# Kernel optimization log

Measured on AMD Instinct MI355X. Metric: run time of the kernel, lower is better.

## Reference

```python
import jax, jax.numpy as jnp
import numpy as np

N = 100_000   # nodes
E = 3_200_000 # edges (avg degree 32)

def _glorot(k, shape):
    fan_in, fan_out = shape
    lim = float(np.sqrt(6.0 / (fan_in + fan_out)))
    return jax.random.uniform(k, shape, jnp.float32, -lim, lim)

def setup_inputs() -> dict:
    key = jax.random.key(0)
    ks = jax.random.split(key, 8)
    x = jax.random.normal(ks[0], (N, 3), dtype=jnp.float32)
    edge_index = jax.random.randint(ks[1], (2, E), 0, N, dtype=jnp.int32)
    choices = jax.random.bernoulli(ks[2], 0.5, (N,))
    W1 = _glorot(ks[3], (3, 16));  b1 = jnp.zeros((16,), jnp.float32)
    W2 = _glorot(ks[4], (16, 16)); b2 = jnp.zeros((16,), jnp.float32)
    W3 = _glorot(ks[5], (16, 1));  b3 = jnp.zeros((1,), jnp.float32)
    fc_w = _glorot(ks[6], (16, 1)); fc_b = jnp.zeros((1,), jnp.float32)
    return dict(x=x, edge_index=edge_index, choices=choices,
                W1=W1, b1=b1, W2=W2, b2=b2, W3=W3, b3=b3,
                fc_w=fc_w, fc_b=fc_b)

def reference(x, edge_index, choices, W1, b1, W2, b2, W3, b3, fc_w, fc_b):
    row, col = edge_index[0], edge_index[1]  # source -> target
    # improved=True GCN norm: self-loop weight 2, deg = in_degree + 2
    deg = jax.ops.segment_sum(jnp.ones((E,), x.dtype), col, num_segments=N) + 2.0
    dinv = jax.lax.rsqrt(deg)                    # [N]
    enorm = dinv[row] * dinv[col]                # [E] edge normalization
    self_norm = 2.0 * dinv * dinv                # [N] self-loop term

    def gcn(h, W, b):
        h = h @ W                                # [N, F_out]
        agg = jax.ops.segment_sum(h[row] * enorm[:, None], col, num_segments=N)
        return agg + self_norm[:, None] * h + b

    h = jax.nn.relu(gcn(x, W1, b1))
    h = jax.nn.relu(gcn(h, W2, b2))
    c = gcn(h, W3, b3)[:, 0]                     # [N] per-node logit
    # masked softmax over chosen nodes (torch masked_select + softmax,
    # expressed with static shape: non-chosen entries get probability 0)
    logits = jnp.where(choices, c, -jnp.inf)
    choice = jax.nn.softmax(logits, axis=0)      # [N]
    # global_mean_pool with a single graph = mean over all nodes
    v = jnp.mean(h, axis=0, keepdims=True)       # [1, 16]
    value = v @ fc_w + fc_b                      # [1, 1]
    return choice, value
```

## Files before the change

kernel.cpp:

```cpp
#include <hip/hip_runtime.h>
#include <hip/hip_fp16.h>
#include <math.h>

#define BLK 256


#define BSH 8
#define NB 512
#define CAP 10240
#define SCAP 11264
#define EB 8192
#define BINTH 512

__device__ inline float4 load_h4(const __half* base, int node, int sub) {
    const uint2* p = reinterpret_cast<const uint2*>(base + ((size_t)node << 4)) + sub;
    uint2 u = *p;
    union { unsigned u; __half2 h; } a, b;
    a.u = u.x; b.u = u.y;
    float2 fa = __half22float2(a.h), fb = __half22float2(b.h);
    return make_float4(fa.x, fa.y, fb.x, fb.y);
}

__device__ inline void store_h4(__half* base, int node, int sub, float4 v) {
    union { unsigned u; __half2 h; } a, b;
    a.h = __floats2half2_rn(v.x, v.y);
    b.h = __floats2half2_rn(v.z, v.w);
    uint2 u; u.x = a.u; u.y = b.u;
    *(reinterpret_cast<uint2*>(base + ((size_t)node << 4)) + sub) = u;
}

__device__ inline float3 load_xs(const __half* xs, int node) {
    uint2 u = *reinterpret_cast<const uint2*>(xs + ((size_t)node << 2));
    union { unsigned u; __half2 h; } a, b;
    a.u = u.x; b.u = u.y;
    float2 fa = __half22float2(a.h), fb = __half22float2(b.h);
    return make_float3(fa.x, fa.y, fb.x);
}

__global__ void k_init(int* __restrict__ gcur, float* __restrict__ scal) {
    int t = threadIdx.x;
    gcur[t] = 0;
    if (t < 18) scal[t] = 0.f;
}

__global__ void __launch_bounds__(BINTH) k_bin(const int* __restrict__ row,
                                               const int* __restrict__ col,
                                               int* __restrict__ gcur,
                                               int* __restrict__ packed, int E) {
    __shared__ int stage[EB];
    __shared__ unsigned short sbuk[EB];
    __shared__ int hist[NB];
    __shared__ int lscan[NB];
    __shared__ int cur[NB];
    __shared__ int gbase[NB];
    int tid = threadIdx.x;
    int base = blockIdx.x * EB;
    int cnt = min(EB, E - base);

    hist[tid] = 0;
    __syncthreads();
    for (int j = tid; j < cnt; j += BINTH) {
        int c = __builtin_nontemporal_load(col + base + j);
        atomicAdd(&hist[c >> BSH], 1);
    }
    __syncthreads();
    lscan[tid] = hist[tid];
    __syncthreads();
    for (int d = 1; d < NB; d <<= 1) {
        int t = (tid >= d) ? lscan[tid - d] : 0;
        __syncthreads();
        if (tid >= d) lscan[tid] += t;
        __syncthreads();
    }
    {
        int ex = lscan[tid] - hist[tid];
        lscan[tid] = ex;
        cur[tid] = ex;
    }
    __syncthreads();
    for (int j = tid; j < cnt; j += BINTH) {
        int c = __builtin_nontemporal_load(col + base + j);
        int r = __builtin_nontemporal_load(row + base + j);
        int b = c >> BSH;
        int p = atomicAdd(&cur[b], 1);
        stage[p] = (r << BSH) | (c & ((1 << BSH) - 1));
        sbuk[p] = (unsigned short)b;
    }
    __syncthreads();
    if (hist[tid] > 0) gbase[tid] = tid * CAP + atomicAdd(&gcur[tid], hist[tid]);
    __syncthreads();
    for (int j = tid; j < cnt; j += BINTH) {
        int b = sbuk[j];
        int pos = gbase[b] + (j - lscan[b]);
        packed[pos] = stage[j];
    }
}

__global__ void __launch_bounds__(BLK) k_place(const int* __restrict__ packed,
                                               const int* __restrict__ bcnt,
                                               const float* __restrict__ x,
                                               int* __restrict__ degi,
                                               int* __restrict__ offs,
                                               float* __restrict__ dinv,
                                               __half* __restrict__ xs,
                                               int* __restrict__ srcs, int n) {
    __shared__ int cnt[256];
    __shared__ int lcur[256];
    __shared__ int ssum[256];
    int tid = threadIdx.x;
    int b = blockIdx.x;
    int nb0 = b << BSH;
    cnt[tid] = 0;
    __syncthreads();
    int ecnt = bcnt[b];
    const int* pk = packed + (size_t)b * CAP;
    for (int j = tid; j < ecnt; j += BLK)
        atomicAdd(&cnt[pk[j] & 255], 1);
    __syncthreads();
    int c = cnt[tid];
    int pl = (c + 3) & ~3;
    ssum[tid] = pl;
    __syncthreads();
    for (int d = 1; d < 256; d <<= 1) {
        int t = (tid >= d) ? ssum[tid - d] : 0;
        __syncthreads();
        if (tid >= d) ssum[tid] += t;
        __syncthreads();
    }
    int A = b * SCAP + (ssum[tid] - pl);
    lcur[tid] = A;
    int valid = min(n - nb0, 256);
    int i = nb0 + tid;
    if (tid < valid) {
        degi[i] = pl;
        offs[i] = A;
        float di = rsqrtf((float)c + 2.0f);
        dinv[i] = di;
        float x0 = x[i * 3 + 0], x1 = x[i * 3 + 1], x2 = x[i * 3 + 2];
        union { unsigned u; __half2 h; } a2, b2;
        a2.h = __floats2half2_rn(di * x0, di * x1);
        b2.h = __floats2half2_rn(di * x2, 0.f);
        uint2 u; u.x = a2.u; u.y = b2.u;
        *reinterpret_cast<uint2*>(xs + ((size_t)i << 2)) = u;
        for (int k = c; k < pl; k++) srcs[A + k] = n;
    }
    if (b == 0 && tid == 0) {
        uint2 z; z.x = 0u; z.y = 0u;
        *reinterpret_cast<uint2*>(xs + ((size_t)n << 2)) = z;
    }
    __syncthreads();
    for (int j = tid; j < ecnt; j += BLK) {
        int v = pk[j];
        int li = v & 255;
        int slot = atomicAdd(&lcur[li], 1);
        srcs[slot] = v >> BSH;
    }
}

__global__ void __launch_bounds__(BLK) k_agg1(const __half* __restrict__ xs,
                                              const int* __restrict__ offs,
                                              const int* __restrict__ degi,
                                              const int* __restrict__ srcs,
                                              const float* __restrict__ dinv,
                                              const float* __restrict__ b1,
                                              const float* __restrict__ W1,
                                              const float* __restrict__ W2,
                                              __half* __restrict__ hwsB, int n) {
    __shared__ float w1[48];
    __shared__ float w2[256];
    __shared__ float bb[16];
    __shared__ float hbuf[64][17];
    int tid = threadIdx.x;
    w2[tid] = W2[tid];
    if (tid < 48) w1[tid] = W1[tid];
    if (tid < 16) bb[tid] = b1[tid];
    if (blockIdx.x == 0 && tid < 8)
        reinterpret_cast<unsigned*>(hwsB + ((size_t)n << 4))[tid] = 0u;
    __syncthreads();
    int nl = tid >> 2, sub = tid & 3;
    int i = blockIdx.x * 64 + nl;
    bool act = (i < n);
    float di = 0.f;
    if (act) {
        di = dinv[i];
        float ax = 0.f, ay = 0.f, az = 0.f;
        float bx = 0.f, by = 0.f, bz = 0.f;
        int A = offs[i], pc = degi[i];
        for (int j = A + 4 * sub; j < A + pc; j += 16) {
            int4 s = *reinterpret_cast<const int4*>(srcs + j);
            float3 q0 = load_xs(xs, s.x);
            float3 q1 = load_xs(xs, s.y);
            float3 q2 = load_xs(xs, s.z);
            float3 q3 = load_xs(xs, s.w);
            ax += q0.x + q1.x; ay += q0.y + q1.y; az += q0.z + q1.z;
            bx += q2.x + q3.x; by += q2.y + q3.y; bz += q2.z + q3.z;
        }
        ax += bx; ay += by; az += bz;
        ax += __shfl_xor(ax, 1); ay += __shfl_xor(ay, 1); az += __shfl_xor(az, 1);
        ax += __shfl_xor(ax, 2); ay += __shfl_xor(ay, 2); az += __shfl_xor(az, 2);
        float3 s = load_xs(xs, i);
        ax += 2.f * s.x; ay += 2.f * s.y; az += 2.f * s.z;
#pragma unroll
        for (int k = 0; k < 4; k++) {
            int f = sub * 4 + k;
            float hv = di * (ax * w1[f] + ay * w1[16 + f] + az * w1[32 + f]) + bb[f];
            hbuf[nl][f] = fmaxf(hv, 0.f);
        }
    }
    __syncthreads();
    if (act) {
        const float* hn = hbuf[nl];
        float s0 = 0.f, s1 = 0.f, s2 = 0.f, s3 = 0.f;
#pragma unroll
        for (int f = 0; f < 16; f++) {
            float hv = hn[f];
            const float4 wq = *(const float4*)&w2[f * 16 + sub * 4];
            s0 += hv * wq.x; s1 += hv * wq.y; s2 += hv * wq.z; s3 += hv * wq.w;
        }
        store_h4(hwsB, i, sub, make_float4(di * s0, di * s1, di * s2, di * s3));
    }
}

#define GATHERV(HWS)                                                            \
    float4 acc;                                                                 \
    {                                                                           \
        float4 s0 = load_h4(HWS, i, sub);                                       \
        acc = make_float4(2.f * s0.x, 2.f * s0.y, 2.f * s0.z, 2.f * s0.w);      \
        float4 a1 = make_float4(0.f, 0.f, 0.f, 0.f);                            \
        float4 a2 = a1, a3 = a1;                                                \
        int A = offs[i], pc = degi[i];                                          \
        int j = A;                                                              \
        for (; j + 8 <= A + pc; j += 8) {                                       \
            int4 sa = *reinterpret_cast<const int4*>(srcs + j);                 \
            int4 sb = *reinterpret_cast<const int4*>(srcs + j + 4);             \
            float4 q0 = load_h4(HWS, sa.x, sub);                                \
            float4 q1 = load_h4(HWS, sa.y, sub);                                \
            float4 q2 = load_h4(HWS, sa.z, sub);                                \
            float4 q3 = load_h4(HWS, sa.w, sub);                                \
            float4 q4 = load_h4(HWS, sb.x, sub);                                \
            float4 q5 = load_h4(HWS, sb.y, sub);                                \
            float4 q6 = load_h4(HWS, sb.z, sub);                                \
            float4 q7 = load_h4(HWS, sb.w, sub);                                \
            acc.x += q0.x + q4.x; acc.y += q0.y + q4.y;                         \
            acc.z += q0.z + q4.z; acc.w += q0.w + q4.w;                         \
            a1.x += q1.x + q5.x; a1.y += q1.y + q5.y;                           \
            a1.z += q1.z + q5.z; a1.w += q1.w + q5.w;                           \
            a2.x += q2.x + q6.x; a2.y += q2.y + q6.y;                           \
            a2.z += q2.z + q6.z; a2.w += q2.w + q6.w;                           \
            a3.x += q3.x + q7.x; a3.y += q3.y + q7.y;                           \
            a3.z += q3.z + q7.z; a3.w += q3.w + q7.w;                           \
        }                                                                       \
        if (j < A + pc) {                   \
            int4 sa = *reinterpret_cast<const int4*>(srcs + j);                 \
            float4 q0 = load_h4(HWS, sa.x, sub);                                \
            float4 q1 = load_h4(HWS, sa.y, sub);                                \
            float4 q2 = load_h4(HWS, sa.z, sub);                                \
            float4 q3 = load_h4(HWS, sa.w, sub);                                \
            acc.x += q0.x; acc.y += q0.y; acc.z += q0.z; acc.w += q0.w;         \
            a1.x += q1.x; a1.y += q1.y; a1.z += q1.z; a1.w += q1.w;             \
            a2.x += q2.x; a2.y += q2.y; a2.z += q2.z; a2.w += q2.w;             \
            a3.x += q3.x; a3.y += q3.y; a3.z += q3.z; a3.w += q3.w;             \
        }                                                                       \
        acc.x += a1.x + a2.x + a3.x;                                            \
        acc.y += a1.y + a2.y + a3.y;                                            \
        acc.z += a1.z + a2.z + a3.z;                                            \
        acc.w += a1.w + a2.w + a3.w;                                            \
    }

__global__ void __launch_bounds__(BLK) k_agg2(const __half* __restrict__ hwsB,
                                              const int* __restrict__ offs,
                                              const int* __restrict__ degi,
                                              const int* __restrict__ srcs,
                                              const float* __restrict__ dinv,
                                              const float* __restrict__ b2,
                                              const float* __restrict__ W3,
                                              float* __restrict__ hws3,
                                              float* __restrict__ pool, int n) {
    __shared__ float w3[16];
    __shared__ float bb[16];
    __shared__ float lp[16];
    int tid = threadIdx.x;
    if (tid < 16) { w3[tid] = W3[tid]; bb[tid] = b2[tid]; lp[tid] = 0.f; }
    if (blockIdx.x == 0 && tid == 0) hws3[n] = 0.f;
    __syncthreads();
    int nl = tid >> 2, sub = tid & 3;
    int i = blockIdx.x * 64 + nl;
    bool act = (i < n);
    float4 h = make_float4(0.f, 0.f, 0.f, 0.f);
    if (act) {
        float di = dinv[i];
        GATHERV(hwsB);
        h.x = fmaxf(di * acc.x + bb[sub * 4 + 0], 0.f);
        h.y = fmaxf(di * acc.y + bb[sub * 4 + 1], 0.f);
        h.z = fmaxf(di * acc.z + bb[sub * 4 + 2], 0.f);
        h.w = fmaxf(di * acc.w + bb[sub * 4 + 3], 0.f);
        float p = h.x * w3[sub * 4 + 0] + h.y * w3[sub * 4 + 1]
                + h.z * w3[sub * 4 + 2] + h.w * w3[sub * 4 + 3];
        p += __shfl_xor(p, 1);
        p += __shfl_xor(p, 2);
        if (sub == 0) hws3[i] = di * p;
    }
    float4 hp = h;
#pragma unroll
    for (int m = 4; m < 64; m <<= 1) {
        hp.x += __shfl_xor(hp.x, m);
        hp.y += __shfl_xor(hp.y, m);
        hp.z += __shfl_xor(hp.z, m);
        hp.w += __shfl_xor(hp.w, m);
    }
    if ((tid & 63) < 4) {
        atomicAdd(&lp[sub * 4 + 0], hp.x);
        atomicAdd(&lp[sub * 4 + 1], hp.y);
        atomicAdd(&lp[sub * 4 + 2], hp.z);
        atomicAdd(&lp[sub * 4 + 3], hp.w);
    }
    __syncthreads();
    if (tid < 16) atomicAdd(&pool[tid], lp[tid]);
}

__global__ void __launch_bounds__(BLK) k_agg3(const float* __restrict__ hws3,
                                              const int* __restrict__ offs,
                                              const int* __restrict__ degi,
                                              const int* __restrict__ srcs,
                                              const float* __restrict__ dinv,
                                              const float* __restrict__ b3,
                                              const int* __restrict__ choices,
                                              float* __restrict__ cbuf,
                                              float* __restrict__ bmax,
                                              float* __restrict__ bsum, int n) {
    __shared__ float red[BLK];
    int tid = threadIdx.x;
    int nl = tid >> 2, sub = tid & 3;
    int i = blockIdx.x * 64 + nl;
    bool act = (i < n);
    float s0 = 0.f, s1 = 0.f;
    if (act) {
        int A = offs[i], pc = degi[i];
        for (int j = A + 4 * sub; j < A + pc; j += 16) {
            int4 s = *reinterpret_cast<const int4*>(srcs + j);
            s0 += hws3[s.x] + hws3[s.z];
            s1 += hws3[s.y] + hws3[s.w];
        }
    }
    float s = s0 + s1;
    s += __shfl_xor(s, 1);
    s += __shfl_xor(s, 2);
    float logit = -INFINITY;
    if (act && sub == 0) {
        float c = dinv[i] * (s + 2.f * hws3[i]) + b3[0];
        cbuf[i] = c;
        if (choices[i] != 0) logit = c;
    }
    red[tid] = logit;
    __syncthreads();
    for (int d = BLK / 2; d > 0; d >>= 1) {
        if (tid < d) red[tid] = fmaxf(red[tid], red[tid + d]);
        __syncthreads();
    }
    float bm = red[0];
    __syncthreads();
    red[tid] = (logit > -INFINITY) ? expf(logit - bm) : 0.f;
    __syncthreads();
    for (int d = BLK / 2; d > 0; d >>= 1) {
        if (tid < d) red[tid] += red[tid + d];
        __syncthreads();
    }
    if (tid == 0) { bmax[blockIdx.x] = bm; bsum[blockIdx.x] = red[0]; }
}

__global__ void __launch_bounds__(BLK) k_comb(const float* __restrict__ bmax,
                                              const float* __restrict__ bsum,
                                              float* __restrict__ scal_m,
                                              float* __restrict__ Ssum, int nblk) {
    __shared__ float red[BLK];
    int tid = threadIdx.x;
    float m = -INFINITY;
    for (int i = tid; i < nblk; i += BLK) m = fmaxf(m, bmax[i]);
    red[tid] = m;
    __syncthreads();
    for (int d = BLK / 2; d > 0; d >>= 1) {
        if (tid < d) red[tid] = fmaxf(red[tid], red[tid + d]);
        __syncthreads();
    }
    float M = red[0];
    __syncthreads();
    float s = 0.f;
    for (int i = tid; i < nblk; i += BLK) {
        float bm = bmax[i];
        if (bm > -INFINITY) s += bsum[i] * expf(bm - M);
    }
    red[tid] = s;
    __syncthreads();
    for (int d = BLK / 2; d > 0; d >>= 1) {
        if (tid < d) red[tid] += red[tid + d];
        __syncthreads();
    }
    if (tid == 0) { scal_m[0] = M; Ssum[0] = red[0]; }
}

__global__ void __launch_bounds__(BLK) k_final(const float* __restrict__ cbuf,
                                               const int* __restrict__ choices,
                                               const float* __restrict__ scal_m,
                                               const float* __restrict__ Ssum,
                                               const float* __restrict__ pool,
                                               const float* __restrict__ fcw,
                                               const float* __restrict__ fcb,
                                               float* __restrict__ out, int n) {
    int i = blockIdx.x * BLK + threadIdx.x;
    if (i < n) {
        float p = 0.0f;
        if (choices[i] != 0) {
            float m = scal_m[0], S = Ssum[0];
            p = expf(cbuf[i] - m) / S;
        }
        out[i] = p;
    }
    if (blockIdx.x == 0 && threadIdx.x == 0) {
        float invn = 1.0f / (float)n;
        float v = 0.0f;
#pragma unroll
        for (int f = 0; f < 16; f++) v += (pool[f] * invn) * fcw[f];
        out[n] = v + fcb[0];
    }
}

extern "C" void kernel_launch(void* const* d_in, const int* in_sizes, int n_in,
                              void* d_out, int out_size, void* d_ws, size_t ws_size,
                              hipStream_t stream) {
    const float* x       = (const float*)d_in[0];
    const int*   ei      = (const int*)d_in[1];
    const int*   choices = (const int*)d_in[2];
    const float* W1 = (const float*)d_in[3];
    const float* b1 = (const float*)d_in[4];
    const float* W2 = (const float*)d_in[5];
    const float* b2 = (const float*)d_in[6];
    const float* W3 = (const float*)d_in[7];
    const float* b3 = (const float*)d_in[8];
    const float* fcw = (const float*)d_in[9];
    const float* fcb = (const float*)d_in[10];
    float* out = (float*)d_out;

    int n = in_sizes[0] / 3;
    int E = in_sizes[1] / 2;
    const int* row = ei;
    const int* col = ei + E;

    int nblkN = (n + BLK - 1) / BLK;
    int nblk64 = (n + 63) / 64;
    int nbuck = (n + (1 << BSH) - 1) >> BSH;
    int nblkBin = (E + EB - 1) / EB;

    char* ws = (char*)d_ws;
    size_t o = 0;
    auto alloc = [&](size_t bytes) { char* p = ws + o; o += (bytes + 15) & ~(size_t)15; return p; };
    int*   degi   = (int*)  alloc((size_t)n * 4);
    int*   offs   = (int*)  alloc((size_t)n * 4);
    float* dinv   = (float*)alloc((size_t)n * 4);
    float* hws3   = (float*)alloc((size_t)(n + 1) * 4);
    float* cbuf   = (float*)alloc((size_t)n * 4);
    float* bmax   = (float*)alloc(8192);
    float* bsum   = (float*)alloc(8192);
    int*   gcur   = (int*)  alloc(NB * 4);
    float* scal   = (float*)alloc(256);
    float* Ssum   = scal + 0;
    float* pool   = scal + 1;
    float* scal_m = scal + 17;
    __half* xs    = (__half*)alloc((size_t)(n + 1) * 4 * 2);
    size_t hw_bytes = (size_t)(n + 1) * 16 * 2;
    size_t pk_bytes = (size_t)NB * CAP * 4;
    char*  blob   = alloc(hw_bytes > pk_bytes ? hw_bytes : pk_bytes);
    int*    packed = (int*)blob;
    __half* hwsB   = (__half*)blob;
    int*   srcs   = (int*)  alloc((size_t)NB * SCAP * 4);
    (void)ws_size;

    k_init<<<1, NB, 0, stream>>>(gcur, scal);
    k_bin<<<nblkBin, BINTH, 0, stream>>>(row, col, gcur, packed, E);
    k_place<<<nbuck, BLK, 0, stream>>>(packed, gcur, x, degi, offs, dinv, xs, srcs, n);

    k_agg1<<<nblk64, BLK, 0, stream>>>(xs, offs, degi, srcs, dinv, b1, W1, W2, hwsB, n);
    k_agg2<<<nblk64, BLK, 0, stream>>>(hwsB, offs, degi, srcs, dinv, b2, W3, hws3, pool, n);
    k_agg3<<<nblk64, BLK, 0, stream>>>(hws3, offs, degi, srcs, dinv, b3, choices, cbuf, bmax, bsum, n);

    k_comb<<<1, BLK, 0, stream>>>(bmax, bsum, scal_m, Ssum, nblk64);
    k_final<<<nblkN, BLK, 0, stream>>>(cbuf, choices, scal_m, Ssum, pool, fcw, fcb, out, n);
}
```

Measured before the change: 232.8 us.

## Process two nodes per thread group in aggregation and fold softmax combine into final

Aggregation kernels for layers 2 and 3 now handle two nodes per 4-lane group. Their gather loops are interleaved with sentinel padding so that more independent loads are in flight per thread. Neighbor lists are padded to multiples of 8, with a larger per-bucket capacity, so the 8-wide loop needs no tail handling. The separate single-block softmax combine kernel is removed, and every block of the final kernel recomputes the global max and sum itself. This saves one launch at the cost of redundant per-block reduction work and extra padded gathers.

```diff
diff --git a/kernel.cpp b/kernel.cpp
--- a/kernel.cpp
+++ b/kernel.cpp
@@ -8,7 +8,7 @@
 #define BSH 8
 #define NB 512
 #define CAP 10240
-#define SCAP 11264
+#define SCAP 12288
 #define EB 8192
 #define BINTH 512
 
@@ -118,7 +118,7 @@
         atomicAdd(&cnt[pk[j] & 255], 1);
     __syncthreads();
     int c = cnt[tid];
-    int pl = (c + 3) & ~3;
+    int pl = (c + 7) & ~7;
     ssum[tid] = pl;
     __syncthreads();
     for (int d = 1; d < 256; d <<= 1) {
@@ -221,52 +221,6 @@
     }
 }
 
-#define GATHERV(HWS)                                                            \
-    float4 acc;                                                                 \
-    {                                                                           \
-        float4 s0 = load_h4(HWS, i, sub);                                       \
-        acc = make_float4(2.f * s0.x, 2.f * s0.y, 2.f * s0.z, 2.f * s0.w);      \
-        float4 a1 = make_float4(0.f, 0.f, 0.f, 0.f);                            \
-        float4 a2 = a1, a3 = a1;                                                \
-        int A = offs[i], pc = degi[i];                                          \
-        int j = A;                                                              \
-        for (; j + 8 <= A + pc; j += 8) {                                       \
-            int4 sa = *reinterpret_cast<const int4*>(srcs + j);                 \
-            int4 sb = *reinterpret_cast<const int4*>(srcs + j + 4);             \
-            float4 q0 = load_h4(HWS, sa.x, sub);                                \
-            float4 q1 = load_h4(HWS, sa.y, sub);                                \
-            float4 q2 = load_h4(HWS, sa.z, sub);                                \
-            float4 q3 = load_h4(HWS, sa.w, sub);                                \
-            float4 q4 = load_h4(HWS, sb.x, sub);                                \
-            float4 q5 = load_h4(HWS, sb.y, sub);                                \
-            float4 q6 = load_h4(HWS, sb.z, sub);                                \
-            float4 q7 = load_h4(HWS, sb.w, sub);                                \
-            acc.x += q0.x + q4.x; acc.y += q0.y + q4.y;                         \
-            acc.z += q0.z + q4.z; acc.w += q0.w + q4.w;                         \
-            a1.x += q1.x + q5.x; a1.y += q1.y + q5.y;                           \
-            a1.z += q1.z + q5.z; a1.w += q1.w + q5.w;                           \
-            a2.x += q2.x + q6.x; a2.y += q2.y + q6.y;                           \
-            a2.z += q2.z + q6.z; a2.w += q2.w + q6.w;                           \
-            a3.x += q3.x + q7.x; a3.y += q3.y + q7.y;                           \
-            a3.z += q3.z + q7.z; a3.w += q3.w + q7.w;                           \
-        }                                                                       \
-        if (j < A + pc) {                   \
-            int4 sa = *reinterpret_cast<const int4*>(srcs + j);                 \
-            float4 q0 = load_h4(HWS, sa.x, sub);                                \
-            float4 q1 = load_h4(HWS, sa.y, sub);                                \
-            float4 q2 = load_h4(HWS, sa.z, sub);                                \
-            float4 q3 = load_h4(HWS, sa.w, sub);                                \
-            acc.x += q0.x; acc.y += q0.y; acc.z += q0.z; acc.w += q0.w;         \
-            a1.x += q1.x; a1.y += q1.y; a1.z += q1.z; a1.w += q1.w;             \
-            a2.x += q2.x; a2.y += q2.y; a2.z += q2.z; a2.w += q2.w;             \
-            a3.x += q3.x; a3.y += q3.y; a3.z += q3.z; a3.w += q3.w;             \
-        }                                                                       \
-        acc.x += a1.x + a2.x + a3.x;                                            \
-        acc.y += a1.y + a2.y + a3.y;                                            \
-        acc.z += a1.z + a2.z + a3.z;                                            \
-        acc.w += a1.w + a2.w + a3.w;                                            \
-    }
-
 __global__ void __launch_bounds__(BLK) k_agg2(const __half* __restrict__ hwsB,
                                               const int* __restrict__ offs,
                                               const int* __restrict__ degi,
@@ -284,23 +238,90 @@
     if (blockIdx.x == 0 && tid == 0) hws3[n] = 0.f;
     __syncthreads();
     int nl = tid >> 2, sub = tid & 3;
-    int i = blockIdx.x * 64 + nl;
-    bool act = (i < n);
-    float4 h = make_float4(0.f, 0.f, 0.f, 0.f);
-    if (act) {
-        float di = dinv[i];
-        GATHERV(hwsB);
-        h.x = fmaxf(di * acc.x + bb[sub * 4 + 0], 0.f);
-        h.y = fmaxf(di * acc.y + bb[sub * 4 + 1], 0.f);
-        h.z = fmaxf(di * acc.z + bb[sub * 4 + 2], 0.f);
-        h.w = fmaxf(di * acc.w + bb[sub * 4 + 3], 0.f);
-        float p = h.x * w3[sub * 4 + 0] + h.y * w3[sub * 4 + 1]
-                + h.z * w3[sub * 4 + 2] + h.w * w3[sub * 4 + 3];
-        p += __shfl_xor(p, 1);
-        p += __shfl_xor(p, 2);
-        if (sub == 0) hws3[i] = di * p;
-    }
-    float4 hp = h;
+    int iA = blockIdx.x * 128 + nl;
+    int iB = iA + 64;
+    bool actA = (iA < n), actB = (iB < n);
+    float diA = actA ? dinv[iA] : 0.f;
+    float diB = actB ? dinv[iB] : 0.f;
+    int AA = actA ? offs[iA] : 0;
+    int AB = actB ? offs[iB] : 0;
+    int plA = actA ? degi[iA] : 0;
+    int plB = actB ? degi[iB] : 0;
+    float4 z4 = make_float4(0.f, 0.f, 0.f, 0.f);
+    float4 sA = actA ? load_h4(hwsB, iA, sub) : z4;
+    float4 sB = actB ? load_h4(hwsB, iB, sub) : z4;
+    float4 accA = make_float4(2.f * sA.x, 2.f * sA.y, 2.f * sA.z, 2.f * sA.w);
+    float4 accB = make_float4(2.f * sB.x, 2.f * sB.y, 2.f * sB.z, 2.f * sB.w);
+    float4 a1A = z4, a1B = z4;
+    int plM = max(plA, plB);
+    for (int j = 0; j < plM; j += 8) {
+        int ja = min(j, max(plA - 8, 0));
+        int jb = min(j, max(plB - 8, 0));
+        int4 sa0 = *reinterpret_cast<const int4*>(srcs + AA + ja);
+        int4 sa1 = *reinterpret_cast<const int4*>(srcs + AA + ja + 4);
+        int4 sb0 = *reinterpret_cast<const int4*>(srcs + AB + jb);
+        int4 sb1 = *reinterpret_cast<const int4*>(srcs + AB + jb + 4);
+        if (j >= plA) { sa0 = make_int4(n, n, n, n); sa1 = sa0; }
+        if (j >= plB) { sb0 = make_int4(n, n, n, n); sb1 = sb0; }
+        float4 qa0 = load_h4(hwsB, sa0.x, sub);
+        float4 qa1 = load_h4(hwsB, sa0.y, sub);
+        float4 qa2 = load_h4(hwsB, sa0.z, sub);
+        float4 qa3 = load_h4(hwsB, sa0.w, sub);
+        float4 qa4 = load_h4(hwsB, sa1.x, sub);
+        float4 qa5 = load_h4(hwsB, sa1.y, sub);
+        float4 qa6 = load_h4(hwsB, sa1.z, sub);
+        float4 qa7 = load_h4(hwsB, sa1.w, sub);
+        float4 qb0 = load_h4(hwsB, sb0.x, sub);
+        float4 qb1 = load_h4(hwsB, sb0.y, sub);
+        float4 qb2 = load_h4(hwsB, sb0.z, sub);
+        float4 qb3 = load_h4(hwsB, sb0.w, sub);
+        float4 qb4 = load_h4(hwsB, sb1.x, sub);
+        float4 qb5 = load_h4(hwsB, sb1.y, sub);
+        float4 qb6 = load_h4(hwsB, sb1.z, sub);
+        float4 qb7 = load_h4(hwsB, sb1.w, sub);
+        accA.x += qa0.x + qa2.x + qa4.x + qa6.x;
+        accA.y += qa0.y + qa2.y + qa4.y + qa6.y;
+        accA.z += qa0.z + qa2.z + qa4.z + qa6.z;
+        accA.w += qa0.w + qa2.w + qa4.w + qa6.w;
+        a1A.x += qa1.x + qa3.x + qa5.x + qa7.x;
+        a1A.y += qa1.y + qa3.y + qa5.y + qa7.y;
+        a1A.z += qa1.z + qa3.z + qa5.z + qa7.z;
+        a1A.w += qa1.w + qa3.w + qa5.w + qa7.w;
+        accB.x += qb0.x + qb2.x + qb4.x + qb6.x;
+        accB.y += qb0.y + qb2.y + qb4.y + qb6.y;
+        accB.z += qb0.z + qb2.z + qb4.z + qb6.z;
+        accB.w += qb0.w + qb2.w + qb4.w + qb6.w;
+        a1B.x += qb1.x + qb3.x + qb5.x + qb7.x;
+        a1B.y += qb1.y + qb3.y + qb5.y + qb7.y;
+        a1B.z += qb1.z + qb3.z + qb5.z + qb7.z;
+        a1B.w += qb1.w + qb3.w + qb5.w + qb7.w;
+    }
+    accA.x += a1A.x; accA.y += a1A.y; accA.z += a1A.z; accA.w += a1A.w;
+    accB.x += a1B.x; accB.y += a1B.y; accB.z += a1B.z; accB.w += a1B.w;
+    float4 hA = z4, hB = z4;
+    if (actA) {
+        hA.x = fmaxf(diA * accA.x + bb[sub * 4 + 0], 0.f);
+        hA.y = fmaxf(diA * accA.y + bb[sub * 4 + 1], 0.f);
+        hA.z = fmaxf(diA * accA.z + bb[sub * 4 + 2], 0.f);
+        hA.w = fmaxf(diA * accA.w + bb[sub * 4 + 3], 0.f);
+    }
+    if (actB) {
+        hB.x = fmaxf(diB * accB.x + bb[sub * 4 + 0], 0.f);
+        hB.y = fmaxf(diB * accB.y + bb[sub * 4 + 1], 0.f);
+        hB.z = fmaxf(diB * accB.z + bb[sub * 4 + 2], 0.f);
+        hB.w = fmaxf(diB * accB.w + bb[sub * 4 + 3], 0.f);
+    }
+    float pA = hA.x * w3[sub * 4 + 0] + hA.y * w3[sub * 4 + 1]
+             + hA.z * w3[sub * 4 + 2] + hA.w * w3[sub * 4 + 3];
+    float pB = hB.x * w3[sub * 4 + 0] + hB.y * w3[sub * 4 + 1]
+             + hB.z * w3[sub * 4 + 2] + hB.w * w3[sub * 4 + 3];
+    pA += __shfl_xor(pA, 1); pA += __shfl_xor(pA, 2);
+    pB += __shfl_xor(pB, 1); pB += __shfl_xor(pB, 2);
+    if (sub == 0) {
+        if (actA) hws3[iA] = diA * pA;
+        if (actB) hws3[iB] = diB * pB;
+    }
+    float4 hp = make_float4(hA.x + hB.x, hA.y + hB.y, hA.z + hB.z, hA.w + hB.w);
 #pragma unroll
     for (int m = 4; m < 64; m <<= 1) {
         hp.x += __shfl_xor(hp.x, m);
@@ -331,27 +352,44 @@
     __shared__ float red[BLK];
     int tid = threadIdx.x;
     int nl = tid >> 2, sub = tid & 3;
-    int i = blockIdx.x * 64 + nl;
-    bool act = (i < n);
-    float s0 = 0.f, s1 = 0.f;
-    if (act) {
-        int A = offs[i], pc = degi[i];
-        for (int j = A + 4 * sub; j < A + pc; j += 16) {
-            int4 s = *reinterpret_cast<const int4*>(srcs + j);
-            s0 += hws3[s.x] + hws3[s.z];
-            s1 += hws3[s.y] + hws3[s.w];
+    int iA = blockIdx.x * 128 + nl;
+    int iB = iA + 64;
+    bool actA = (iA < n), actB = (iB < n);
+    int AA = actA ? offs[iA] : 0;
+    int AB = actB ? offs[iB] : 0;
+    int plA = actA ? degi[iA] : 0;
+    int plB = actB ? degi[iB] : 0;
+    float sA0 = 0.f, sA1 = 0.f, sB0 = 0.f, sB1 = 0.f;
+    int plM = max(plA, plB);
+    for (int j = 4 * sub; j < plM; j += 16) {
+        int ja = min(j, max(plA - 4, 0));
+        int jb = min(j, max(plB - 4, 0));
+        int4 sa = *reinterpret_cast<const int4*>(srcs + AA + ja);
+        int4 sb = *reinterpret_cast<const int4*>(srcs + AB + jb);
+        if (j >= plA) sa = make_int4(n, n, n, n);
+        if (j >= plB) sb = make_int4(n, n, n, n);
+        sA0 += hws3[sa.x] + hws3[sa.z];
+        sA1 += hws3[sa.y] + hws3[sa.w];
+        sB0 += hws3[sb.x] + hws3[sb.z];
+        sB1 += hws3[sb.y] + hws3[sb.w];
+    }
+    float sA = sA0 + sA1, sB = sB0 + sB1;
+    sA += __shfl_xor(sA, 1); sA += __shfl_xor(sA, 2);
+    sB += __shfl_xor(sB, 1); sB += __shfl_xor(sB, 2);
+    float lA = -INFINITY, lB = -INFINITY;
+    if (sub == 0) {
+        if (actA) {
+            float c = dinv[iA] * (sA + 2.f * hws3[iA]) + b3[0];
+            cbuf[iA] = c;
+            if (choices[iA] != 0) lA = c;
         }
-    }
-    float s = s0 + s1;
-    s += __shfl_xor(s, 1);
-    s += __shfl_xor(s, 2);
-    float logit = -INFINITY;
-    if (act && sub == 0) {
-        float c = dinv[i] * (s + 2.f * hws3[i]) + b3[0];
-        cbuf[i] = c;
-        if (choices[i] != 0) logit = c;
-    }
-    red[tid] = logit;
+        if (actB) {
+            float c = dinv[iB] * (sB + 2.f * hws3[iB]) + b3[0];
+            cbuf[iB] = c;
+            if (choices[iB] != 0) lB = c;
+        }
+    }
+    red[tid] = fmaxf(lA, lB);
     __syncthreads();
     for (int d = BLK / 2; d > 0; d >>= 1) {
         if (tid < d) red[tid] = fmaxf(red[tid], red[tid + d]);
@@ -359,7 +397,10 @@
     }
     float bm = red[0];
     __syncthreads();
-    red[tid] = (logit > -INFINITY) ? expf(logit - bm) : 0.f;
+    float es = 0.f;
+    if (lA > -INFINITY) es += expf(lA - bm);
+    if (lB > -INFINITY) es += expf(lB - bm);
+    red[tid] = es;
     __syncthreads();
     for (int d = BLK / 2; d > 0; d >>= 1) {
         if (tid < d) red[tid] += red[tid + d];
@@ -368,11 +409,17 @@
     if (tid == 0) { bmax[blockIdx.x] = bm; bsum[blockIdx.x] = red[0]; }
 }
 
-__global__ void __launch_bounds__(BLK) k_comb(const float* __restrict__ bmax,
-                                              const float* __restrict__ bsum,
-                                              float* __restrict__ scal_m,
-                                              float* __restrict__ Ssum, int nblk) {
+__global__ void __launch_bounds__(BLK) k_final(const float* __restrict__ cbuf,
+                                               const int* __restrict__ choices,
+                                               const float* __restrict__ bmax,
+                                               const float* __restrict__ bsum,
+                                               const float* __restrict__ pool,
+                                               const float* __restrict__ fcw,
+                                               const float* __restrict__ fcb,
+                                               float* __restrict__ out,
+                                               int nblk, int n) {
     __shared__ float red[BLK];
+    __shared__ float MS[2];
     int tid = threadIdx.x;
     float m = -INFINITY;
     for (int i = tid; i < nblk; i += BLK) m = fmaxf(m, bmax[i]);
@@ -395,27 +442,16 @@
         if (tid < d) red[tid] += red[tid + d];
         __syncthreads();
     }
-    if (tid == 0) { scal_m[0] = M; Ssum[0] = red[0]; }
-}
-
-__global__ void __launch_bounds__(BLK) k_final(const float* __restrict__ cbuf,
-                                               const int* __restrict__ choices,
-                                               const float* __restrict__ scal_m,
-                                               const float* __restrict__ Ssum,
-                                               const float* __restrict__ pool,
-                                               const float* __restrict__ fcw,
-                                               const float* __restrict__ fcb,
-                                               float* __restrict__ out, int n) {
-    int i = blockIdx.x * BLK + threadIdx.x;
+    if (tid == 0) { MS[0] = M; MS[1] = red[0]; }
+    __syncthreads();
+    float Mv = MS[0], Sv = MS[1];
+    int i = blockIdx.x * BLK + tid;
     if (i < n) {
         float p = 0.0f;
-        if (choices[i] != 0) {
-            float m = scal_m[0], S = Ssum[0];
-            p = expf(cbuf[i] - m) / S;
-        }
+        if (choices[i] != 0) p = expf(cbuf[i] - Mv) / Sv;
         out[i] = p;
     }
-    if (blockIdx.x == 0 && threadIdx.x == 0) {
+    if (blockIdx.x == 0 && tid == 0) {
         float invn = 1.0f / (float)n;
         float v = 0.0f;
 #pragma unroll
@@ -447,6 +483,7 @@
 
     int nblkN = (n + BLK - 1) / BLK;
     int nblk64 = (n + 63) / 64;
+    int nblk128 = (n + 127) / 128;
     int nbuck = (n + (1 << BSH) - 1) >> BSH;
     int nblkBin = (E + EB - 1) / EB;
 
@@ -462,9 +499,7 @@
     float* bsum   = (float*)alloc(8192);
     int*   gcur   = (int*)  alloc(NB * 4);
     float* scal   = (float*)alloc(256);
-    float* Ssum   = scal + 0;
     float* pool   = scal + 1;
-    float* scal_m = scal + 17;
     __half* xs    = (__half*)alloc((size_t)(n + 1) * 4 * 2);
     size_t hw_bytes = (size_t)(n + 1) * 16 * 2;
     size_t pk_bytes = (size_t)NB * CAP * 4;
@@ -479,9 +514,8 @@
     k_place<<<nbuck, BLK, 0, stream>>>(packed, gcur, x, degi, offs, dinv, xs, srcs, n);
 
     k_agg1<<<nblk64, BLK, 0, stream>>>(xs, offs, degi, srcs, dinv, b1, W1, W2, hwsB, n);
-    k_agg2<<<nblk64, BLK, 0, stream>>>(hwsB, offs, degi, srcs, dinv, b2, W3, hws3, pool, n);
-    k_agg3<<<nblk64, BLK, 0, stream>>>(hws3, offs, degi, srcs, dinv, b3, choices, cbuf, bmax, bsum, n);
-
-    k_comb<<<1, BLK, 0, stream>>>(bmax, bsum, scal_m, Ssum, nblk64);
-    k_final<<<nblkN, BLK, 0, stream>>>(cbuf, choices, scal_m, Ssum, pool, fcw, fcb, out, n);
-}
+    k_agg2<<<nblk128, BLK, 0, stream>>>(hwsB, offs, degi, srcs, dinv, b2, W3, hws3, pool, n);
+    k_agg3<<<nblk128, BLK, 0, stream>>>(hws3, offs, degi, srcs, dinv, b3, choices, cbuf, bmax, bsum, n);
+
+    k_final<<<nblkN, BLK, 0, stream>>>(cbuf, choices, bmax, bsum, pool, fcw, fcb, out, nblk128, n);
+}
```

Measured after the change: 225.8 us. 3.0% less time.
